# Optimization experiments

Hardware: AMD Instinct MI355X
Metric: run time of the kernel (lower is better)

Reference implementation:

```python
import jax, jax.numpy as jnp
import numpy as np

B, T, X, E, H, L = 4096, 32, 256, 32, 512, 2  # batch, theta_size, x_size, n_masks, hidden, num_hidden_layers


def _prelu(v, a):
    # PReLU with per-channel slope a (broadcast [E,H] or [B,E,H] vs [B,E,H])
    return jnp.where(v >= 0, v, a * v)


def setup_inputs() -> dict:
    key = jax.random.key(0)
    ks = jax.random.split(key, 12)
    theta = jax.random.normal(ks[0], (B, T), dtype=jnp.float32)
    x = jax.random.normal(ks[1], (B, X), dtype=jnp.float32)
    masks = jax.random.randint(ks[2], (E, T), 0, 2, dtype=jnp.int32)
    masks = masks.at[:, 0].set(1)  # guarantee non-empty subsets
    D = T + X
    s_in = 1.0 / np.sqrt(D)
    s_h = 1.0 / np.sqrt(H)
    # first Linear, split into theta-part and x-part of the weight matrix
    W1t = jax.random.normal(ks[3], (E, T, H), dtype=jnp.float32) * s_in
    W1x = jax.random.normal(ks[4], (E, X, H), dtype=jnp.float32) * s_in
    b1 = jax.random.normal(ks[5], (E, H), dtype=jnp.float32) * s_in
    a1 = jnp.full((E, H), 0.25, dtype=jnp.float32)  # PReLU init
    # num_layers hidden Linear(H,H) + PReLU
    Wh = jax.random.normal(ks[6], (L, E, H, H), dtype=jnp.float32) * s_h
    bh = jax.random.normal(ks[7], (L, E, H), dtype=jnp.float32) * s_h
    ah = jnp.full((L, E, H), 0.25, dtype=jnp.float32)
    # output Linear(H, 1) -> squeeze(-1)
    Wo = jax.random.normal(ks[8], (E, H), dtype=jnp.float32) * s_h
    bo = jax.random.normal(ks[9], (E,), dtype=jnp.float32) * s_h
    return {"theta": theta, "x": x, "masks": masks, "W1t": W1t, "W1x": W1x,
            "b1": b1, "a1": a1, "Wh": Wh, "bh": bh, "ah": ah, "Wo": Wo, "bo": bo}


def reference(theta, x, masks, W1t, W1x, b1, a1, Wh, bh, ah, Wo, bo):
    # theta[..., mask] followed by Linear is equivalent to masking theta per
    # expert and contracting with the full per-expert theta weight block.
    m = masks.astype(theta.dtype)                      # [E, T]
    tm = theta[:, None, :] * m[None, :, :]             # [B, E, T]
    h = (jnp.einsum('bet,eth->beh', tm, W1t)
         + jnp.einsum('bx,exh->beh', x, W1x) + b1)     # [B, E, H]
    h = _prelu(h, a1)
    for i in range(Wh.shape[0]):                       # small fixed layer loop
        h = jnp.einsum('beh,ehk->bek', h, Wh[i]) + bh[i]
        h = _prelu(h, ah[i])
    # Linear(H,1).squeeze(-1), stacked over masks on the last dim -> [B, E]
    return jnp.einsum('beh,eh->be', h, Wo) + bo
```

## Files before the change

kernel.cpp:

```cpp
#include <hip/hip_runtime.h>
#include <stdint.h>

#define B_SZ 4096
#define T_SZ 32
#define X_SZ 256
#define E_SZ 32
#define H_SZ 512
#define BM   64
#define AROW 1040

typedef __attribute__((ext_vector_type(8))) short  short8;
typedef __attribute__((ext_vector_type(4))) float  floatx4;

__device__ __forceinline__ unsigned short f2bf(float f) {
  unsigned u = __float_as_uint(f);
  u += 0x7fffu + ((u >> 16) & 1u);
  return (unsigned short)(u >> 16);
}
__device__ __forceinline__ unsigned pk2(float a, float b) {
  return (unsigned)f2bf(a) | ((unsigned)f2bf(b) << 16);
}

__global__ __launch_bounds__(256) void prep_kernel(
    const float* __restrict__ W1t, const float* __restrict__ W1x,
    const int* __restrict__ masks, const float* __restrict__ Wh,
    uint4* __restrict__ wcat, uint4* __restrict__ whf) {
  int gid = blockIdx.x * 256 + threadIdx.x;
  const int NU1 = E_SZ * 9 * 2048;
  if (gid < NU1) {
    int c  = gid >> 11;
    int u  = gid & 2047;
    int e  = c / 9, kt = c - e * 9;
    int nb = u >> 6, l = u & 63;
    int n  = nb * 16 + (l & 15);
    int k0 = kt * 32 + (l >> 4) * 8;
    unsigned r[4];
#pragma unroll
    for (int p = 0; p < 4; ++p) {
      int   k  = k0 + p * 2;
      float v0 = (k < T_SZ)
                     ? W1t[(e * T_SZ + k) * H_SZ + n] * (float)masks[e * T_SZ + k]
                     : W1x[(e * X_SZ + (k - T_SZ)) * H_SZ + n];
      int   k1 = k + 1;
      float v1 = (k1 < T_SZ)
                     ? W1t[(e * T_SZ + k1) * H_SZ + n] * (float)masks[e * T_SZ + k1]
                     : W1x[(e * X_SZ + (k1 - T_SZ)) * H_SZ + n];
      r[p] = pk2(v0, v1);
    }
    wcat[gid] = make_uint4(r[0], r[1], r[2], r[3]);
  } else {
    int g  = gid - NU1;
    int c  = g >> 11;
    int u  = g & 2047;
    int kt = c & 15, le = c >> 4;
    int nb = u >> 6, l = u & 63;
    int n  = nb * 16 + (l & 15);
    int k0 = kt * 32 + (l >> 4) * 8;
    const float* base = Wh + (size_t)le * H_SZ * H_SZ + n;
    unsigned r[4];
#pragma unroll
    for (int p = 0; p < 4; ++p) {
      float v0 = base[(size_t)(k0 + p * 2) * H_SZ];
      float v1 = base[(size_t)(k0 + p * 2 + 1) * H_SZ];
      r[p] = pk2(v0, v1);
    }
    whf[g] = make_uint4(r[0], r[1], r[2], r[3]);
  }
}

__global__ __launch_bounds__(512, 4) void mlp_kernel(
    const float* __restrict__ theta, const float* __restrict__ x,
    const short8* __restrict__ wcat, const short8* __restrict__ whf,
    const float* __restrict__ b1, const float* __restrict__ a1,
    const float* __restrict__ bh, const float* __restrict__ ah,
    const float* __restrict__ Wo, const float* __restrict__ bo,
    float* __restrict__ out) {
  __shared__ __align__(16) char smA[BM * AROW];
  const int tid = threadIdx.x;
  const int bid = blockIdx.x;
  const int r5  = bid & 31;
  const int e   = (r5 & 7) * 4 + (r5 >> 3);
  const int m0  = (bid >> 5) * BM;
  const int w   = tid >> 6, l = tid & 63, l16 = l & 15, quad = l >> 4;

  {
    int r = tid >> 3, c = tid & 7;
    float4 th = *(const float4*)(theta + (size_t)(m0 + r) * T_SZ + c * 4);
    *(uint2*)(smA + r * AROW + c * 8) = make_uint2(pk2(th.x, th.y), pk2(th.z, th.w));
    const float4* xp = (const float4*)(x + (size_t)(m0 + r) * X_SZ + c * 32);
#pragma unroll
    for (int q = 0; q < 4; ++q) {
      float4 a = xp[q * 2], b = xp[q * 2 + 1];
      *(uint4*)(smA + r * AROW + 64 + c * 64 + q * 16) =
          make_uint4(pk2(a.x, a.y), pk2(a.z, a.w), pk2(b.x, b.y), pk2(b.z, b.w));
    }
  }
  __syncthreads();

  floatx4 acc[4][4];

  auto gemm = [&](const short8* wbase, int nkt) {
#pragma unroll
    for (int mb = 0; mb < 4; ++mb)
#pragma unroll
      for (int i = 0; i < 4; ++i) acc[mb][i] = (floatx4)(0.f);
    short8 bcur[4], bnxt[4];
    const int boff = w * 256 + l;
#pragma unroll
    for (int i = 0; i < 4; ++i) bcur[i] = wbase[boff + i * 64];
    for (int kt = 0; kt < nkt; ++kt) {
      const short8* wn = wbase + (size_t)(kt + 1 < nkt ? kt + 1 : kt) * 2048;
#pragma unroll
      for (int i = 0; i < 4; ++i) bnxt[i] = wn[boff + i * 64];
      short8 af[4];
#pragma unroll
      for (int mb = 0; mb < 4; ++mb)
        af[mb] = *(const short8*)(smA + (mb * 16 + l16) * AROW + kt * 64 + quad * 16);
#pragma unroll
      for (int mb = 0; mb < 4; ++mb)
#pragma unroll
        for (int i = 0; i < 4; ++i)
          acc[mb][i] = __builtin_amdgcn_mfma_f32_16x16x32_bf16(af[mb], bcur[i],
                                                               acc[mb][i], 0, 0, 0);
#pragma unroll
      for (int i = 0; i < 4; ++i) bcur[i] = bnxt[i];
    }
  };

  auto epi_store = [&](const float* bias, const float* slope) {
    float bb[4], aa[4];
#pragma unroll
    for (int i = 0; i < 4; ++i) {
      int col = w * 64 + i * 16 + l16;
      bb[i] = bias[col];
      aa[i] = slope[col];
    }
    __syncthreads();
#pragma unroll
    for (int mb = 0; mb < 4; ++mb) {
#pragma unroll
      for (int i = 0; i < 4; ++i) {
        unsigned dw[4];
#pragma unroll
        for (int r = 0; r < 4; ++r) {
          float v = acc[mb][i][r] + bb[i];
          v = v >= 0.f ? v : aa[i] * v;
          float o  = __shfl_xor(v, 1, 64);
          float lo = (l16 & 1) ? o : v;
          float hi = (l16 & 1) ? v : o;
          dw[r] = pk2(lo, hi);
        }
        int col2  = w * 64 + i * 16 + (l16 & ~1);
        int rbase = (l16 & 1) * 2;
#pragma unroll
        for (int rr = 0; rr < 2; ++rr) {
          int row = mb * 16 + quad * 4 + rbase + rr;
          *(unsigned*)(smA + row * AROW + col2 * 2) = dw[rbase + rr];
        }
      }
    }
    __syncthreads();
  };

  gemm(wcat + (size_t)e * 9 * 2048, 9);
  epi_store(b1 + (size_t)e * H_SZ, a1 + (size_t)e * H_SZ);
  gemm(whf + (size_t)e * 16 * 2048, 16);
  epi_store(bh + (size_t)e * H_SZ, ah + (size_t)e * H_SZ);
  gemm(whf + (size_t)(E_SZ + e) * 16 * 2048, 16);
  {
    float bb[4], aa[4], wo[4];
#pragma unroll
    for (int i = 0; i < 4; ++i) {
      int col = w * 64 + i * 16 + l16;
      bb[i] = bh[(size_t)(E_SZ + e) * H_SZ + col];
      aa[i] = ah[(size_t)(E_SZ + e) * H_SZ + col];
      wo[i] = Wo[(size_t)e * H_SZ + col];
    }
    float ps[4][4];
#pragma unroll
    for (int mb = 0; mb < 4; ++mb)
#pragma unroll
      for (int r = 0; r < 4; ++r) ps[mb][r] = 0.f;
#pragma unroll
    for (int mb = 0; mb < 4; ++mb)
#pragma unroll
      for (int i = 0; i < 4; ++i)
#pragma unroll
        for (int r = 0; r < 4; ++r) {
          float v = acc[mb][i][r] + bb[i];
          v = v >= 0.f ? v : aa[i] * v;
          ps[mb][r] += v * wo[i];
        }
#pragma unroll
    for (int d = 1; d < 16; d <<= 1)
#pragma unroll
      for (int mb = 0; mb < 4; ++mb)
#pragma unroll
        for (int r = 0; r < 4; ++r) ps[mb][r] += __shfl_xor(ps[mb][r], d, 64);
    __syncthreads();
    float* scratch = (float*)smA;
    if (l16 == 0) {
#pragma unroll
      for (int mb = 0; mb < 4; ++mb)
#pragma unroll
        for (int r = 0; r < 4; ++r)
          scratch[(mb * 16 + quad * 4 + r) * 8 + w] = ps[mb][r];
    }
    __syncthreads();
    if (tid < BM) {
      float s = 0.f;
#pragma unroll
      for (int ww = 0; ww < 8; ++ww) s += scratch[tid * 8 + ww];
      out[(size_t)(m0 + tid) * E_SZ + e] = s + bo[e];
    }
  }
}

extern "C" void kernel_launch(void* const* d_in, const int* in_sizes, int n_in,
                              void* d_out, int out_size, void* d_ws, size_t ws_size,
                              hipStream_t stream) {
  const float* theta = (const float*)d_in[0];
  const float* x     = (const float*)d_in[1];
  const int*   masks = (const int*)d_in[2];
  const float* W1t   = (const float*)d_in[3];
  const float* W1x   = (const float*)d_in[4];
  const float* b1    = (const float*)d_in[5];
  const float* a1    = (const float*)d_in[6];
  const float* Wh    = (const float*)d_in[7];
  const float* bh    = (const float*)d_in[8];
  const float* ah    = (const float*)d_in[9];
  const float* Wo    = (const float*)d_in[10];
  const float* bo    = (const float*)d_in[11];
  float* out = (float*)d_out;

  uint4* wcat = (uint4*)d_ws;
  uint4* whf  = (uint4*)((char*)d_ws + (size_t)E_SZ * 9 * 2048 * 16);

  prep_kernel<<<10496, 256, 0, stream>>>(W1t, W1x, masks, Wh, wcat, whf);
  mlp_kernel<<<2048, 512, 0, stream>>>(theta, x, (const short8*)wcat,
                                       (const short8*)whf, b1, a1, bh, ah, Wo, bo,
                                       out);
}
```

Baseline: 319.5 us.

## Stage weight repacking through LDS and double-buffer MFMA weight loads

The weight prep kernel now reads each 32-row k-tile with coalesced float4 loads, converts to bf16 into a padded LDS tile, and then emits the MFMA fragment layout from LDS. The old version gathered strided scalar columns straight from global memory. The x-tile load into shared memory is reordered so adjacent threads read contiguous chunks. The GEMM loop is unrolled by two with ping-pong weight register buffers, removing the per-iteration register copy so loads overlap better with MFMA work.

After: 349.6 us. 1.09x slower.

```diff
diff --git a/kernel.cpp b/kernel.cpp
--- a/kernel.cpp
+++ b/kernel.cpp
@@ -21,50 +21,61 @@
   return (unsigned)f2bf(a) | ((unsigned)f2bf(b) << 16);
 }
 
-__global__ __launch_bounds__(256) void prep_kernel(
+#define LPITCH 524
+
+__global__ __launch_bounds__(256) void prep2_kernel(
     const float* __restrict__ W1t, const float* __restrict__ W1x,
     const int* __restrict__ masks, const float* __restrict__ Wh,
     uint4* __restrict__ wcat, uint4* __restrict__ whf) {
-  int gid = blockIdx.x * 256 + threadIdx.x;
-  const int NU1 = E_SZ * 9 * 2048;
-  if (gid < NU1) {
-    int c  = gid >> 11;
-    int u  = gid & 2047;
-    int e  = c / 9, kt = c - e * 9;
+  __shared__ unsigned short lds[32 * LPITCH];
+  const int b = blockIdx.x, t = threadIdx.x;
+  const bool l1 = b < 288;
+  int e = 0, kt;
+  const float* hbase = nullptr;
+  if (l1) {
+    e  = b / 9;
+    kt = b - e * 9;
+  } else {
+    int g = b - 288;
+    kt = g & 15;
+    hbase = Wh + (size_t)(g >> 4) * H_SZ * H_SZ + (size_t)kt * 32 * H_SZ;
+  }
+#pragma unroll 4
+  for (int p = 0; p < 16; ++p) {
+    int f  = p * 256 + t;
+    int kk = f >> 7, n = (f & 127) * 4;
+    float4 v;
+    if (l1) {
+      int k = kt * 32 + kk;
+      if (k < T_SZ) {
+        v = *(const float4*)(W1t + ((size_t)e * T_SZ + k) * H_SZ + n);
+        float m = (float)masks[e * T_SZ + k];
+        v.x *= m; v.y *= m; v.z *= m; v.w *= m;
+      } else {
+        v = *(const float4*)(W1x + ((size_t)e * X_SZ + (k - T_SZ)) * H_SZ + n);
+      }
+    } else {
+      v = *(const float4*)(hbase + (size_t)kk * H_SZ + n);
+    }
+    *(uint2*)&lds[kk * LPITCH + n] = make_uint2(pk2(v.x, v.y), pk2(v.z, v.w));
+  }
+  __syncthreads();
+  uint4* dst = l1 ? (wcat + ((size_t)e * 9 + kt) * 2048)
+                  : (whf + (size_t)(b - 288) * 2048);
+#pragma unroll 2
+  for (int p = 0; p < 8; ++p) {
+    int u  = p * 256 + t;
     int nb = u >> 6, l = u & 63;
     int n  = nb * 16 + (l & 15);
-    int k0 = kt * 32 + (l >> 4) * 8;
-    unsigned r[4];
-#pragma unroll
-    for (int p = 0; p < 4; ++p) {
-      int   k  = k0 + p * 2;
-      float v0 = (k < T_SZ)
-                     ? W1t[(e * T_SZ + k) * H_SZ + n] * (float)masks[e * T_SZ + k]
-                     : W1x[(e * X_SZ + (k - T_SZ)) * H_SZ + n];
-      int   k1 = k + 1;
-      float v1 = (k1 < T_SZ)
-                     ? W1t[(e * T_SZ + k1) * H_SZ + n] * (float)masks[e * T_SZ + k1]
-                     : W1x[(e * X_SZ + (k1 - T_SZ)) * H_SZ + n];
-      r[p] = pk2(v0, v1);
-    }
-    wcat[gid] = make_uint4(r[0], r[1], r[2], r[3]);
-  } else {
-    int g  = gid - NU1;
-    int c  = g >> 11;
-    int u  = g & 2047;
-    int kt = c & 15, le = c >> 4;
-    int nb = u >> 6, l = u & 63;
-    int n  = nb * 16 + (l & 15);
-    int k0 = kt * 32 + (l >> 4) * 8;
-    const float* base = Wh + (size_t)le * H_SZ * H_SZ + n;
-    unsigned r[4];
-#pragma unroll
-    for (int p = 0; p < 4; ++p) {
-      float v0 = base[(size_t)(k0 + p * 2) * H_SZ];
-      float v1 = base[(size_t)(k0 + p * 2 + 1) * H_SZ];
-      r[p] = pk2(v0, v1);
-    }
-    whf[g] = make_uint4(r[0], r[1], r[2], r[3]);
+    int k0 = (l >> 4) * 8;
+    unsigned d[4];
+#pragma unroll
+    for (int j = 0; j < 4; ++j) {
+      unsigned lo = lds[(k0 + 2 * j)     * LPITCH + n];
+      unsigned hi = lds[(k0 + 2 * j + 1) * LPITCH + n];
+      d[j] = lo | (hi << 16);
+    }
+    dst[u] = make_uint4(d[0], d[1], d[2], d[3]);
   }
 }
 
@@ -87,12 +98,13 @@
     int r = tid >> 3, c = tid & 7;
     float4 th = *(const float4*)(theta + (size_t)(m0 + r) * T_SZ + c * 4);
     *(uint2*)(smA + r * AROW + c * 8) = make_uint2(pk2(th.x, th.y), pk2(th.z, th.w));
-    const float4* xp = (const float4*)(x + (size_t)(m0 + r) * X_SZ + c * 32);
+    const float4* xp = (const float4*)(x + (size_t)(m0 + r) * X_SZ);
 #pragma unroll
     for (int q = 0; q < 4; ++q) {
-      float4 a = xp[q * 2], b = xp[q * 2 + 1];
-      *(uint4*)(smA + r * AROW + 64 + c * 64 + q * 16) =
-          make_uint4(pk2(a.x, a.y), pk2(a.z, a.w), pk2(b.x, b.y), pk2(b.z, b.w));
+      int ch = q * 8 + c;
+      float4 a = xp[ch * 2], bv = xp[ch * 2 + 1];
+      *(uint4*)(smA + r * AROW + 64 + ch * 16) =
+          make_uint4(pk2(a.x, a.y), pk2(a.z, a.w), pk2(bv.x, bv.y), pk2(bv.z, bv.w));
     }
   }
   __syncthreads();
@@ -104,27 +116,34 @@
     for (int mb = 0; mb < 4; ++mb)
 #pragma unroll
       for (int i = 0; i < 4; ++i) acc[mb][i] = (floatx4)(0.f);
-    short8 bcur[4], bnxt[4];
-    const int boff = w * 256 + l;
-#pragma unroll
-    for (int i = 0; i < 4; ++i) bcur[i] = wbase[boff + i * 64];
-    for (int kt = 0; kt < nkt; ++kt) {
-      const short8* wn = wbase + (size_t)(kt + 1 < nkt ? kt + 1 : kt) * 2048;
-#pragma unroll
-      for (int i = 0; i < 4; ++i) bnxt[i] = wn[boff + i * 64];
+    const short8* wp = wbase + w * 256 + l;
+    short8 b0[4], b1v[4];
+#pragma unroll
+    for (int i = 0; i < 4; ++i) b0[i] = wp[i * 64];
+    auto step = [&](const short8* bc, int ktt) {
       short8 af[4];
 #pragma unroll
       for (int mb = 0; mb < 4; ++mb)
-        af[mb] = *(const short8*)(smA + (mb * 16 + l16) * AROW + kt * 64 + quad * 16);
+        af[mb] = *(const short8*)(smA + (mb * 16 + l16) * AROW + ktt * 64 + quad * 16);
 #pragma unroll
       for (int mb = 0; mb < 4; ++mb)
 #pragma unroll
         for (int i = 0; i < 4; ++i)
-          acc[mb][i] = __builtin_amdgcn_mfma_f32_16x16x32_bf16(af[mb], bcur[i],
+          acc[mb][i] = __builtin_amdgcn_mfma_f32_16x16x32_bf16(af[mb], bc[i],
                                                                acc[mb][i], 0, 0, 0);
-#pragma unroll
-      for (int i = 0; i < 4; ++i) bcur[i] = bnxt[i];
-    }
+    };
+    int kt = 0;
+    while (kt + 2 <= nkt) {
+#pragma unroll
+      for (int i = 0; i < 4; ++i) b1v[i] = wp[(size_t)(kt + 1) * 2048 + i * 64];
+      step(b0, kt);
+      int k2 = (kt + 2 < nkt) ? kt + 2 : nkt - 1;
+#pragma unroll
+      for (int i = 0; i < 4; ++i) b0[i] = wp[(size_t)k2 * 2048 + i * 64];
+      step(b1v, kt + 1);
+      kt += 2;
+    }
+    if (kt < nkt) step(b0, kt);
   };
 
   auto epi_store = [&](const float* bias, const float* slope) {
@@ -236,7 +255,7 @@
   uint4* wcat = (uint4*)d_ws;
   uint4* whf  = (uint4*)((char*)d_ws + (size_t)E_SZ * 9 * 2048 * 16);
 
-  prep_kernel<<<10496, 256, 0, stream>>>(W1t, W1x, masks, Wh, wcat, whf);
+  prep2_kernel<<<1312, 256, 0, stream>>>(W1t, W1x, masks, Wh, wcat, whf);
   mlp_kernel<<<2048, 512, 0, stream>>>(theta, x, (const short8*)wcat,
                                        (const short8*)whf, b1, a1, bh, ah, Wo, bo,
                                        out);
```
